# Kernel optimization log

Hardware: AMD Instinct MI355X
Metric: run time of the kernel (lower is better)

Reference implementation:

```python
import jax, jax.numpy as jnp
import numpy as np


def setup_inputs() -> dict:
    key = jax.random.key(0)
    ks = jax.random.split(key, 7)
    B, T, D, H = 32, 2048, 512, 512
    s = 1.0 / np.sqrt(H)
    return {
        "input": jax.random.normal(ks[0], (B, T, D), dtype=jnp.float32),
        "h0": jax.random.normal(ks[1], (B, H), dtype=jnp.float32),
        "c0": jax.random.normal(ks[2], (B, H), dtype=jnp.float32),
        "W_ih": jax.random.normal(ks[3], (4 * H, D), dtype=jnp.float32) * s,
        "W_hh": jax.random.normal(ks[4], (4 * H, H), dtype=jnp.float32) * s,
        "b_ih": jax.random.normal(ks[5], (4 * H,), dtype=jnp.float32) * s,
        "b_hh": jax.random.normal(ks[6], (4 * H,), dtype=jnp.float32) * s,
    }


def _lstm(input, h0, c0, W_ih, W_hh, b_ih, b_hh):
    H = h0.shape[-1]
    # Precompute input projections for all timesteps: [T, B, 4H]
    x_proj = jnp.einsum('btd,gd->tbg', input, W_ih) + b_ih + b_hh

    def step(carry, xp):
        h, c = carry
        gates = xp + h @ W_hh.T  # [B, 4H]
        i, f, g, o = jnp.split(gates, 4, axis=-1)  # PyTorch gate order
        i = jax.nn.sigmoid(i)
        f = jax.nn.sigmoid(f)
        g = jnp.tanh(g)
        o = jax.nn.sigmoid(o)
        c_new = f * c + i * g
        h_new = o * jnp.tanh(c_new)
        return (h_new, c_new), None

    (h, c), _ = jax.lax.scan(step, (h0, c0), x_proj)
    return h, c


def reference(input, h0, c0, W_ih, W_hh, b_ih, b_hh):
    return _lstm(input, h0, c0, W_ih, W_hh, b_ih, b_hh)
```

## Files before the change

kernel.cpp:

```cpp
#include <hip/hip_runtime.h>

#define B_ 32
#define T_ 2048
#define D_ 512
#define H_ 512
#define G4 2048
#define NWG 64

typedef short short8 __attribute__((ext_vector_type(8)));
typedef float floatv16 __attribute__((ext_vector_type(16)));
typedef float floatv4 __attribute__((ext_vector_type(4)));

static __device__ __forceinline__ unsigned short f2bf(float f) {
  union { float f; unsigned u; } v; v.f = f;
  unsigned u = v.u;
  u += 0x7fffu + ((u >> 16) & 1u);
  return (unsigned short)(u >> 16);
}
static __device__ __forceinline__ float bf2f(unsigned short h) {
  union { unsigned u; float f; } v; v.u = ((unsigned)h) << 16;
  return v.f;
}
static __device__ __forceinline__ float sigm(float x) { return 1.0f / (1.0f + __expf(-x)); }
static __device__ __forceinline__ float tanh_(float x) {
  float e = __expf(-2.0f * fabsf(x));
  float t = (1.0f - e) / (1.0f + e);
  return copysignf(t, x);
}

#define MFMA32(A, Bv, C) __builtin_amdgcn_mfma_f32_32x32x16_bf16((A), (Bv), (C), 0, 0, 0)

__global__ __launch_bounds__(256) void cvt_kernel(
    const float* __restrict__ Wih, const float* __restrict__ Whh,
    const float* __restrict__ bih, const float* __restrict__ bhh,
    const float* __restrict__ h0, const float* __restrict__ c0,
    short* __restrict__ wih_hi, short* __restrict__ wih_lo, short* __restrict__ whh_hi,
    float* __restrict__ bias, short* __restrict__ hbuf0, float* __restrict__ cws) {
  int i = blockIdx.x * 256 + threadIdx.x;
  if (i < G4 * D_) {
    float w = Wih[i];
    unsigned short hi = f2bf(w);
    wih_hi[i] = (short)hi;
    wih_lo[i] = (short)f2bf(w - bf2f(hi));
    whh_hi[i] = (short)f2bf(Whh[i]);
  }
  if (i < G4) bias[i] = bih[i] + bhh[i];
  if (i < B_ * H_) { hbuf0[i] = (short)f2bf(h0[i]); cws[i] = c0[i]; }
}

__global__ __launch_bounds__(256, 1) void xproj_kernel(
    const float* __restrict__ input,
    const short* __restrict__ wih_hi, const short* __restrict__ wih_lo,
    const float* __restrict__ bias, float* __restrict__ xp, int t0, int TC) {
  __shared__ short xlo_lds[4 * 8192];
  const int tid = threadIdx.x;
  const int wv = tid >> 6, l = tid & 63;
  const int wid = blockIdx.x * 4 + wv;
  const int lt = wid >> 3, nb = wid & 7;
  const int t = t0 + lt;
  const int lb = l & 31, hb = l >> 5;
  const float* xrow = input + ((size_t)lb * T_ + t) * D_ + hb * 8;
  short* slo = xlo_lds + wv * 8192;
  short8 xhi[32];
#pragma unroll
  for (int kb = 0; kb < 32; ++kb) {
    floatv4 x0 = *(const floatv4*)(xrow + kb * 16);
    floatv4 x1 = *(const floatv4*)(xrow + kb * 16 + 4);
    float xs[8] = {x0[0], x0[1], x0[2], x0[3], x1[0], x1[1], x1[2], x1[3]};
    short8 hi, lo;
#pragma unroll
    for (int j = 0; j < 8; ++j) {
      unsigned short h = f2bf(xs[j]);
      hi[j] = (short)h;
      lo[j] = (short)f2bf(xs[j] - bf2f(h));
    }
    xhi[kb] = hi;
    *(short8*)(slo + (kb * 64 + l) * 8) = lo;
  }
  for (int nt = 0; nt < 8; ++nt) {
    const int n0 = nb * 256 + nt * 32;
    const short* whbase = wih_hi + (size_t)(n0 + lb) * D_ + hb * 8;
    const short* wlbase = wih_lo + (size_t)(n0 + lb) * D_ + hb * 8;
    floatv16 a0, a1;
#pragma unroll
    for (int i = 0; i < 16; ++i) { a0[i] = 0.0f; a1[i] = 0.0f; }
#pragma unroll
    for (int kb = 0; kb < 32; ++kb) {
      short8 whi = *(const short8*)(whbase + kb * 16);
      short8 wlo = *(const short8*)(wlbase + kb * 16);
      short8 xl = *(const short8*)(slo + (kb * 64 + l) * 8);
      a0 = MFMA32(whi, xhi[kb], a0);
      a1 = MFMA32(whi, xl, a1);
      a1 = MFMA32(wlo, xhi[kb], a1);
    }
#pragma unroll
    for (int r = 0; r < 16; ++r) {
      int row = (r & 3) + 8 * (r >> 2) + 4 * hb;
      int n = n0 + row;
      xp[((size_t)lt * G4 + n) * B_ + lb] = a0[r] + a1[r] + bias[n];
    }
  }
}

__global__ __launch_bounds__(64, 1) void lstm_rec(
    const float* __restrict__ xp, const short* __restrict__ whh,
    short* __restrict__ hbuf, float* __restrict__ cws, int* __restrict__ flags,
    float* __restrict__ out, int t0, int TC, int writeOut) {
  const int w = blockIdx.x;
  const int l = threadIdx.x;
  const int lb = l & 31, hb = l >> 5;
  const int nl = lb;
  const int ngl = (nl >> 3) * H_ + w * 8 + (nl & 7);
  short8 Wf[32];
#pragma unroll
  for (int kb = 0; kb < 32; ++kb)
    Wf[kb] = *(const short8*)(whh + (size_t)ngl * H_ + kb * 16 + hb * 8);
  float c4[4], h4[4];
#pragma unroll
  for (int q = 0; q < 4; ++q) c4[q] = cws[lb * H_ + w * 8 + 4 * hb + q];

  for (int t = t0; t < t0 + TC; ++t) {
    const float* xpt = xp + (size_t)(t - t0) * G4 * B_;
    float xpv[16];
#pragma unroll
    for (int g = 0; g < 4; ++g)
#pragma unroll
      for (int q = 0; q < 4; ++q)
        xpv[g * 4 + q] = xpt[(size_t)(g * H_ + w * 8 + 4 * hb + q) * B_ + lb];

    if (t > 0) {
      int v;
      do {
        v = __hip_atomic_load(flags + l * 16, __ATOMIC_ACQUIRE, __HIP_MEMORY_SCOPE_AGENT);
      } while (!__all(v >= t));
    }

    const short* hsrc = hbuf + (t & 1) * (B_ * H_) + lb * H_ + hb * 8;
    floatv16 D0, D1;
#pragma unroll
    for (int i = 0; i < 16; ++i) { D0[i] = 0.0f; D1[i] = 0.0f; }
#pragma unroll
    for (int kb = 0; kb < 32; kb += 2) {
      short8 hf0 = *(const short8*)(hsrc + kb * 16);
      short8 hf1 = *(const short8*)(hsrc + kb * 16 + 16);
      D0 = MFMA32(Wf[kb], hf0, D0);
      D1 = MFMA32(Wf[kb + 1], hf1, D1);
    }

    union { unsigned short s[4]; unsigned long long u; } pk;
#pragma unroll
    for (int q = 0; q < 4; ++q) {
      float gi = D0[q] + D1[q] + xpv[q];
      float gf = D0[4 + q] + D1[4 + q] + xpv[4 + q];
      float gg = D0[8 + q] + D1[8 + q] + xpv[8 + q];
      float go = D0[12 + q] + D1[12 + q] + xpv[12 + q];
      float iv = sigm(gi), fv = sigm(gf), gv = tanh_(gg), ov = sigm(go);
      c4[q] = fv * c4[q] + iv * gv;
      h4[q] = ov * tanh_(c4[q]);
      pk.s[q] = f2bf(h4[q]);
    }
    unsigned long long* hdst = (unsigned long long*)(hbuf + ((t + 1) & 1) * (B_ * H_) +
                                                     lb * H_ + w * 8 + 4 * hb);
    __hip_atomic_store(hdst, pk.u, __ATOMIC_RELAXED, __HIP_MEMORY_SCOPE_AGENT);
    if (l == 0)
      __hip_atomic_store(flags + w * 16, t + 1, __ATOMIC_RELEASE, __HIP_MEMORY_SCOPE_AGENT);
  }

#pragma unroll
  for (int q = 0; q < 4; ++q) cws[lb * H_ + w * 8 + 4 * hb + q] = c4[q];
  if (writeOut) {
#pragma unroll
    for (int q = 0; q < 4; ++q) {
      out[lb * H_ + w * 8 + 4 * hb + q] = h4[q];
      out[B_ * H_ + lb * H_ + w * 8 + 4 * hb + q] = c4[q];
    }
  }
}

extern "C" void kernel_launch(void* const* d_in, const int* in_sizes, int n_in,
                              void* d_out, int out_size, void* d_ws, size_t ws_size,
                              hipStream_t stream) {
  (void)in_sizes; (void)n_in; (void)out_size;
  const float* input = (const float*)d_in[0];
  const float* h0 = (const float*)d_in[1];
  const float* c0 = (const float*)d_in[2];
  const float* Wih = (const float*)d_in[3];
  const float* Whh = (const float*)d_in[4];
  const float* bih = (const float*)d_in[5];
  const float* bhh = (const float*)d_in[6];

  char* ws = (char*)d_ws;
  short* wih_hi = (short*)(ws);
  short* wih_lo = (short*)(ws + (2ull << 20));
  short* whh_hi = (short*)(ws + (4ull << 20));
  float* bias = (float*)(ws + (6ull << 20));
  short* hbuf = (short*)(ws + (6ull << 20) + 65536);
  float* cws = (float*)(ws + (6ull << 20) + 131072);
  int* flags = (int*)(ws + (6ull << 20) + 196608);
  float* xp = (float*)(ws + (8ull << 20));

  int TC = 32;
  while (TC < 256 && (8ull << 20) + (size_t)(TC * 2) * (G4 * B_ * 4) <= ws_size) TC <<= 1;

  hipMemsetAsync(flags, 0, 4096, stream);
  cvt_kernel<<<dim3((G4 * D_ + 255) / 256), dim3(256), 0, stream>>>(
      Wih, Whh, bih, bhh, h0, c0, wih_hi, wih_lo, whh_hi, bias, hbuf, cws);
  for (int t0 = 0; t0 < T_; t0 += TC) {
    xproj_kernel<<<dim3(TC * 2), dim3(256), 0, stream>>>(input, wih_hi, wih_lo, bias, xp, t0, TC);
    lstm_rec<<<dim3(NWG), dim3(64), 0, stream>>>(xp, whh_hi, hbuf, cws, flags,
                                                 (float*)d_out, t0, TC,
                                                 (t0 + TC) == T_ ? 1 : 0);
  }
}
```

Before: 13.44 ms.

## Pack recurrence into 8 workgroups of 8 waves with block-level flag sync

The recurrent kernel goes from 64 single-wave workgroups to 8 workgroups of 8 waves each. Each block publishes one flag after a __syncthreads, so each poller reads 8 flags instead of 64. The polling load becomes relaxed with a single acquire fence after the spin loop, and the time-chunk cap rises so fewer kernel launch pairs are needed when workspace allows. The cost is a block barrier every timestep, and the xproj and recurrence phases are still serialized within each chunk.

```diff
diff --git a/kernel.cpp b/kernel.cpp
--- a/kernel.cpp
+++ b/kernel.cpp
@@ -5,7 +5,8 @@
 #define D_ 512
 #define H_ 512
 #define G4 2048
-#define NWG 64
+#define NWG 8
+#define WVW 8
 
 typedef short short8 __attribute__((ext_vector_type(8)));
 typedef float floatv16 __attribute__((ext_vector_type(16)));
@@ -102,22 +103,23 @@
   }
 }
 
-__global__ __launch_bounds__(64, 1) void lstm_rec(
+__global__ __launch_bounds__(512, 2) void lstm_rec(
     const float* __restrict__ xp, const short* __restrict__ whh,
     short* __restrict__ hbuf, float* __restrict__ cws, int* __restrict__ flags,
     float* __restrict__ out, int t0, int TC, int writeOut) {
-  const int w = blockIdx.x;
-  const int l = threadIdx.x;
+  const int wv = threadIdx.x >> 6;
+  const int l = threadIdx.x & 63;
+  const int gw = blockIdx.x * WVW + wv;
   const int lb = l & 31, hb = l >> 5;
   const int nl = lb;
-  const int ngl = (nl >> 3) * H_ + w * 8 + (nl & 7);
+  const int ngl = (nl >> 3) * H_ + gw * 8 + (nl & 7);
   short8 Wf[32];
 #pragma unroll
   for (int kb = 0; kb < 32; ++kb)
     Wf[kb] = *(const short8*)(whh + (size_t)ngl * H_ + kb * 16 + hb * 8);
   float c4[4], h4[4];
 #pragma unroll
-  for (int q = 0; q < 4; ++q) c4[q] = cws[lb * H_ + w * 8 + 4 * hb + q];
+  for (int q = 0; q < 4; ++q) c4[q] = cws[lb * H_ + gw * 8 + 4 * hb + q];
 
   for (int t = t0; t < t0 + TC; ++t) {
     const float* xpt = xp + (size_t)(t - t0) * G4 * B_;
@@ -126,13 +128,14 @@
     for (int g = 0; g < 4; ++g)
 #pragma unroll
       for (int q = 0; q < 4; ++q)
-        xpv[g * 4 + q] = xpt[(size_t)(g * H_ + w * 8 + 4 * hb + q) * B_ + lb];
+        xpv[g * 4 + q] = xpt[(size_t)(g * H_ + gw * 8 + 4 * hb + q) * B_ + lb];
 
     if (t > 0) {
       int v;
       do {
-        v = __hip_atomic_load(flags + l * 16, __ATOMIC_ACQUIRE, __HIP_MEMORY_SCOPE_AGENT);
+        v = __hip_atomic_load(flags + (l & 7) * 16, __ATOMIC_RELAXED, __HIP_MEMORY_SCOPE_AGENT);
       } while (!__all(v >= t));
+      __builtin_amdgcn_fence(__ATOMIC_ACQUIRE, "agent");
     }
 
     const short* hsrc = hbuf + (t & 1) * (B_ * H_) + lb * H_ + hb * 8;
@@ -160,19 +163,20 @@
       pk.s[q] = f2bf(h4[q]);
     }
     unsigned long long* hdst = (unsigned long long*)(hbuf + ((t + 1) & 1) * (B_ * H_) +
-                                                     lb * H_ + w * 8 + 4 * hb);
+                                                     lb * H_ + gw * 8 + 4 * hb);
     __hip_atomic_store(hdst, pk.u, __ATOMIC_RELAXED, __HIP_MEMORY_SCOPE_AGENT);
-    if (l == 0)
-      __hip_atomic_store(flags + w * 16, t + 1, __ATOMIC_RELEASE, __HIP_MEMORY_SCOPE_AGENT);
-  }
-
-#pragma unroll
-  for (int q = 0; q < 4; ++q) cws[lb * H_ + w * 8 + 4 * hb + q] = c4[q];
+    __syncthreads();
+    if (threadIdx.x == 0)
+      __hip_atomic_store(flags + blockIdx.x * 16, t + 1, __ATOMIC_RELEASE, __HIP_MEMORY_SCOPE_AGENT);
+  }
+
+#pragma unroll
+  for (int q = 0; q < 4; ++q) cws[lb * H_ + gw * 8 + 4 * hb + q] = c4[q];
   if (writeOut) {
 #pragma unroll
     for (int q = 0; q < 4; ++q) {
-      out[lb * H_ + w * 8 + 4 * hb + q] = h4[q];
-      out[B_ * H_ + lb * H_ + w * 8 + 4 * hb + q] = c4[q];
+      out[lb * H_ + gw * 8 + 4 * hb + q] = h4[q];
+      out[B_ * H_ + lb * H_ + gw * 8 + 4 * hb + q] = c4[q];
     }
   }
 }
@@ -200,15 +204,16 @@
   float* xp = (float*)(ws + (8ull << 20));
 
   int TC = 32;
-  while (TC < 256 && (8ull << 20) + (size_t)(TC * 2) * (G4 * B_ * 4) <= ws_size) TC <<= 1;
+  while (TC < 2048 && (8ull << 20) + (size_t)(TC * 2) * (G4 * B_ * 4) <= ws_size) TC <<= 1;
 
   hipMemsetAsync(flags, 0, 4096, stream);
   cvt_kernel<<<dim3((G4 * D_ + 255) / 256), dim3(256), 0, stream>>>(
       Wih, Whh, bih, bhh, h0, c0, wih_hi, wih_lo, whh_hi, bias, hbuf, cws);
   for (int t0 = 0; t0 < T_; t0 += TC) {
-    xproj_kernel<<<dim3(TC * 2), dim3(256), 0, stream>>>(input, wih_hi, wih_lo, bias, xp, t0, TC);
-    lstm_rec<<<dim3(NWG), dim3(64), 0, stream>>>(xp, whh_hi, hbuf, cws, flags,
-                                                 (float*)d_out, t0, TC,
-                                                 (t0 + TC) == T_ ? 1 : 0);
-  }
-}
+    int tc = (t0 + TC <= T_) ? TC : (T_ - t0);
+    xproj_kernel<<<dim3(tc * 2), dim3(256), 0, stream>>>(input, wih_hi, wih_lo, bias, xp, t0, tc);
+    lstm_rec<<<dim3(NWG), dim3(512), 0, stream>>>(xp, whh_hi, hbuf, cws, flags,
+                                                  (float*)d_out, t0, tc,
+                                                  (t0 + tc) == T_ ? 1 : 0);
+  }
+}
```

New measurement: 21.63 ms. 60.9% more time.

## Overlap next-chunk input projection with recurrent steps in a fused kernel

Applied to the files above, without the earlier changes.

Fuses the recurrent LSTM kernel and the input-projection GEMM into one launch. 64 blocks run the sequential recurrence for the current time chunk while 192 extra blocks compute the input projections for the next chunk into a double buffer. This hides the projection GEMM behind the latency-bound recurrence instead of running them back to back. The risk is that worker blocks compete with the recurrent blocks for memory bandwidth and CUs, which could slow the spin-wait synchronised critical path.

```diff
diff --git a/kernel.cpp b/kernel.cpp
--- a/kernel.cpp
+++ b/kernel.cpp
@@ -5,7 +5,8 @@
 #define D_ 512
 #define H_ 512
 #define G4 2048
-#define NWG 64
+#define NREC 64
+#define NWRK 192
 
 typedef short short8 __attribute__((ext_vector_type(8)));
 typedef float floatv16 __attribute__((ext_vector_type(16)));
@@ -102,77 +103,130 @@
   }
 }
 
-__global__ __launch_bounds__(64, 1) void lstm_rec(
-    const float* __restrict__ xp, const short* __restrict__ whh,
+__global__ __launch_bounds__(64, 1) void fused_step(
+    const float* __restrict__ input,
+    const short* __restrict__ wih_hi, const short* __restrict__ wih_lo,
+    const float* __restrict__ bias, const short* __restrict__ whh,
     short* __restrict__ hbuf, float* __restrict__ cws, int* __restrict__ flags,
-    float* __restrict__ out, int t0, int TC, int writeOut) {
-  const int w = blockIdx.x;
+    const float* __restrict__ xpc, float* __restrict__ xpn,
+    float* __restrict__ out, int t0, int TC, int writeOut, int doNext) {
+  __shared__ short slo[16384];
   const int l = threadIdx.x;
   const int lb = l & 31, hb = l >> 5;
-  const int nl = lb;
-  const int ngl = (nl >> 3) * H_ + w * 8 + (nl & 7);
-  short8 Wf[32];
-#pragma unroll
-  for (int kb = 0; kb < 32; ++kb)
-    Wf[kb] = *(const short8*)(whh + (size_t)ngl * H_ + kb * 16 + hb * 8);
-  float c4[4], h4[4];
-#pragma unroll
-  for (int q = 0; q < 4; ++q) c4[q] = cws[lb * H_ + w * 8 + 4 * hb + q];
-
-  for (int t = t0; t < t0 + TC; ++t) {
-    const float* xpt = xp + (size_t)(t - t0) * G4 * B_;
-    float xpv[16];
-#pragma unroll
-    for (int g = 0; g < 4; ++g)
-#pragma unroll
-      for (int q = 0; q < 4; ++q)
-        xpv[g * 4 + q] = xpt[(size_t)(g * H_ + w * 8 + 4 * hb + q) * B_ + lb];
-
-    if (t > 0) {
-      int v;
-      do {
-        v = __hip_atomic_load(flags + l * 16, __ATOMIC_ACQUIRE, __HIP_MEMORY_SCOPE_AGENT);
-      } while (!__all(v >= t));
-    }
-
-    const short* hsrc = hbuf + (t & 1) * (B_ * H_) + lb * H_ + hb * 8;
-    floatv16 D0, D1;
-#pragma unroll
-    for (int i = 0; i < 16; ++i) { D0[i] = 0.0f; D1[i] = 0.0f; }
-#pragma unroll
-    for (int kb = 0; kb < 32; kb += 2) {
-      short8 hf0 = *(const short8*)(hsrc + kb * 16);
-      short8 hf1 = *(const short8*)(hsrc + kb * 16 + 16);
-      D0 = MFMA32(Wf[kb], hf0, D0);
-      D1 = MFMA32(Wf[kb + 1], hf1, D1);
-    }
-
-    union { unsigned short s[4]; unsigned long long u; } pk;
-#pragma unroll
-    for (int q = 0; q < 4; ++q) {
-      float gi = D0[q] + D1[q] + xpv[q];
-      float gf = D0[4 + q] + D1[4 + q] + xpv[4 + q];
-      float gg = D0[8 + q] + D1[8 + q] + xpv[8 + q];
-      float go = D0[12 + q] + D1[12 + q] + xpv[12 + q];
-      float iv = sigm(gi), fv = sigm(gf), gv = tanh_(gg), ov = sigm(go);
-      c4[q] = fv * c4[q] + iv * gv;
-      h4[q] = ov * tanh_(c4[q]);
-      pk.s[q] = f2bf(h4[q]);
-    }
-    unsigned long long* hdst = (unsigned long long*)(hbuf + ((t + 1) & 1) * (B_ * H_) +
-                                                     lb * H_ + w * 8 + 4 * hb);
-    __hip_atomic_store(hdst, pk.u, __ATOMIC_RELAXED, __HIP_MEMORY_SCOPE_AGENT);
-    if (l == 0)
-      __hip_atomic_store(flags + w * 16, t + 1, __ATOMIC_RELEASE, __HIP_MEMORY_SCOPE_AGENT);
-  }
-
-#pragma unroll
-  for (int q = 0; q < 4; ++q) cws[lb * H_ + w * 8 + 4 * hb + q] = c4[q];
-  if (writeOut) {
-#pragma unroll
-    for (int q = 0; q < 4; ++q) {
-      out[lb * H_ + w * 8 + 4 * hb + q] = h4[q];
-      out[B_ * H_ + lb * H_ + w * 8 + 4 * hb + q] = c4[q];
+
+  if (blockIdx.x < NREC) {
+    const int w = blockIdx.x;
+    const int ngl = (lb >> 3) * H_ + w * 8 + (lb & 7);
+    short8 Wf[32];
+#pragma unroll
+    for (int kb = 0; kb < 32; ++kb)
+      Wf[kb] = *(const short8*)(whh + (size_t)ngl * H_ + kb * 16 + hb * 8);
+    float c4[4], h4[4];
+#pragma unroll
+    for (int q = 0; q < 4; ++q) c4[q] = cws[lb * H_ + w * 8 + 4 * hb + q];
+
+    for (int t = t0; t < t0 + TC; ++t) {
+      const float* xpt = xpc + (size_t)(t - t0) * G4 * B_;
+      float xpv[16];
+#pragma unroll
+      for (int g = 0; g < 4; ++g)
+#pragma unroll
+        for (int q = 0; q < 4; ++q)
+          xpv[g * 4 + q] = xpt[(size_t)(g * H_ + w * 8 + 4 * hb + q) * B_ + lb];
+
+      if (t > 0) {
+        int v;
+        do {
+          v = __hip_atomic_load(flags + l * 16, __ATOMIC_ACQUIRE, __HIP_MEMORY_SCOPE_AGENT);
+        } while (!__all(v >= t));
+      }
+
+      const short* hsrc = hbuf + (t & 1) * (B_ * H_) + lb * H_ + hb * 8;
+      floatv16 D0, D1;
+#pragma unroll
+      for (int i = 0; i < 16; ++i) { D0[i] = 0.0f; D1[i] = 0.0f; }
+#pragma unroll
+      for (int kb = 0; kb < 32; kb += 2) {
+        short8 hf0 = *(const short8*)(hsrc + kb * 16);
+        short8 hf1 = *(const short8*)(hsrc + kb * 16 + 16);
+        D0 = MFMA32(Wf[kb], hf0, D0);
+        D1 = MFMA32(Wf[kb + 1], hf1, D1);
+      }
+
+      union { unsigned short s[4]; unsigned long long u; } pk;
+#pragma unroll
+      for (int q = 0; q < 4; ++q) {
+        float gi = D0[q] + D1[q] + xpv[q];
+        float gf = D0[4 + q] + D1[4 + q] + xpv[4 + q];
+        float gg = D0[8 + q] + D1[8 + q] + xpv[8 + q];
+        float go = D0[12 + q] + D1[12 + q] + xpv[12 + q];
+        float iv = sigm(gi), fv = sigm(gf), gv = tanh_(gg), ov = sigm(go);
+        c4[q] = fv * c4[q] + iv * gv;
+        h4[q] = ov * tanh_(c4[q]);
+        pk.s[q] = f2bf(h4[q]);
+      }
+      unsigned long long* hdst = (unsigned long long*)(hbuf + ((t + 1) & 1) * (B_ * H_) +
+                                                       lb * H_ + w * 8 + 4 * hb);
+      __hip_atomic_store(hdst, pk.u, __ATOMIC_RELAXED, __HIP_MEMORY_SCOPE_AGENT);
+      if (l == 0)
+        __hip_atomic_store(flags + w * 16, t + 1, __ATOMIC_RELEASE, __HIP_MEMORY_SCOPE_AGENT);
+    }
+
+#pragma unroll
+    for (int q = 0; q < 4; ++q) cws[lb * H_ + w * 8 + 4 * hb + q] = c4[q];
+    if (writeOut) {
+#pragma unroll
+      for (int q = 0; q < 4; ++q) {
+        out[lb * H_ + w * 8 + 4 * hb + q] = h4[q];
+        out[B_ * H_ + lb * H_ + w * 8 + 4 * hb + q] = c4[q];
+      }
+    }
+  } else if (doNext) {
+    const int wkr = blockIdx.x - NREC;
+    const int t0n = t0 + TC;
+    for (int j = wkr; j < TC * 8; j += NWRK) {
+      const int lt = j >> 3, nb = j & 7;
+      const int t = t0n + lt;
+      const float* xrow = input + ((size_t)lb * T_ + t) * D_ + hb * 8;
+      short8 xhi[32];
+#pragma unroll
+      for (int kb = 0; kb < 32; ++kb) {
+        floatv4 x0 = *(const floatv4*)(xrow + kb * 16);
+        floatv4 x1 = *(const floatv4*)(xrow + kb * 16 + 4);
+        float xs[8] = {x0[0], x0[1], x0[2], x0[3], x1[0], x1[1], x1[2], x1[3]};
+        short8 hi, lo;
+#pragma unroll
+        for (int jj = 0; jj < 8; ++jj) {
+          unsigned short h = f2bf(xs[jj]);
+          hi[jj] = (short)h;
+          lo[jj] = (short)f2bf(xs[jj] - bf2f(h));
+        }
+        xhi[kb] = hi;
+        *(short8*)(slo + (kb * 64 + l) * 8) = lo;
+      }
+      for (int nt = 0; nt < 8; ++nt) {
+        const int n0 = nb * 256 + nt * 32;
+        const short* whbase = wih_hi + (size_t)(n0 + lb) * D_ + hb * 8;
+        const short* wlbase = wih_lo + (size_t)(n0 + lb) * D_ + hb * 8;
+        floatv16 a0, a1;
+#pragma unroll
+        for (int i = 0; i < 16; ++i) { a0[i] = 0.0f; a1[i] = 0.0f; }
+#pragma unroll
+        for (int kb = 0; kb < 32; ++kb) {
+          short8 whi = *(const short8*)(whbase + kb * 16);
+          short8 wlo = *(const short8*)(wlbase + kb * 16);
+          short8 xl = *(const short8*)(slo + (kb * 64 + l) * 8);
+          a0 = MFMA32(whi, xhi[kb], a0);
+          a1 = MFMA32(whi, xl, a1);
+          a1 = MFMA32(wlo, xhi[kb], a1);
+        }
+#pragma unroll
+        for (int r = 0; r < 16; ++r) {
+          int row = (r & 3) + 8 * (r >> 2) + 4 * hb;
+          int n = n0 + row;
+          xpn[((size_t)lt * G4 + n) * B_ + lb] = a0[r] + a1[r] + bias[n];
+        }
+      }
     }
   }
 }
@@ -197,18 +251,23 @@
   short* hbuf = (short*)(ws + (6ull << 20) + 65536);
   float* cws = (float*)(ws + (6ull << 20) + 131072);
   int* flags = (int*)(ws + (6ull << 20) + 196608);
-  float* xp = (float*)(ws + (8ull << 20));
 
   int TC = 32;
   while (TC < 256 && (8ull << 20) + (size_t)(TC * 2) * (G4 * B_ * 4) <= ws_size) TC <<= 1;
+  const int nch = T_ / TC;
+  float* xpA = (float*)(ws + (8ull << 20));
+  float* xpB = xpA + (size_t)TC * G4 * B_;
 
   hipMemsetAsync(flags, 0, 4096, stream);
   cvt_kernel<<<dim3((G4 * D_ + 255) / 256), dim3(256), 0, stream>>>(
       Wih, Whh, bih, bhh, h0, c0, wih_hi, wih_lo, whh_hi, bias, hbuf, cws);
-  for (int t0 = 0; t0 < T_; t0 += TC) {
-    xproj_kernel<<<dim3(TC * 2), dim3(256), 0, stream>>>(input, wih_hi, wih_lo, bias, xp, t0, TC);
-    lstm_rec<<<dim3(NWG), dim3(64), 0, stream>>>(xp, whh_hi, hbuf, cws, flags,
-                                                 (float*)d_out, t0, TC,
-                                                 (t0 + TC) == T_ ? 1 : 0);
-  }
-}
+  xproj_kernel<<<dim3(TC * 2), dim3(256), 0, stream>>>(input, wih_hi, wih_lo, bias,
+                                                       xpA, 0, TC);
+  for (int k = 0; k < nch; ++k) {
+    float* cur = (k & 1) ? xpB : xpA;
+    float* nxt = (k & 1) ? xpA : xpB;
+    fused_step<<<dim3(NREC + NWRK), dim3(64), 0, stream>>>(
+        input, wih_hi, wih_lo, bias, whh_hi, hbuf, cws, flags, cur, nxt,
+        (float*)d_out, k * TC, TC, (k == nch - 1) ? 1 : 0, (k < nch - 1) ? 1 : 0);
+  }
+}
```

Result: faster. 12.69 ms (-5.6%).
